# Kernel tuning notes

Hardware: AMD Instinct MI355X
Metric: run time of the kernel (lower is better)

## Reference

```python
import jax, jax.numpy as jnp
import numpy as np

NEG_FILL = -9.0e15
EPS = 1e-7


def setup_inputs() -> dict:
    key = jax.random.key(0)
    k1, k2, k3 = jax.random.split(key, 3)
    N, M, D = 8192, 8192, 256
    feat_x = jax.random.normal(k1, (N, D), dtype=jnp.float32)
    feat_y = jax.random.normal(k2, (M, D), dtype=jnp.float32)
    # Xavier-uniform init for W1 [in_dim, hidden_dim]
    limit = float(np.sqrt(6.0 / (D + D)))
    W1 = jax.random.uniform(k3, (D, D), dtype=jnp.float32, minval=-limit, maxval=limit)
    return {"feat_x": feat_x, "feat_y": feat_y, "W1": W1, "k": 32}


def reference(feat_x, feat_y, W1, k):
    # cosine-style normalization denominators
    norm1 = jnp.linalg.norm(feat_x, axis=1, keepdims=True)      # [N,1]
    norm2 = jnp.linalg.norm(feat_y, axis=1, keepdims=True)      # [M,1]
    # e = (X W1 Y^T) / (norm1 norm2^T + eps)   -> [N, M]
    e = (feat_x @ W1) @ feat_y.T
    e = e / (norm1 * norm2.T + EPS)
    # topk per row, scatter into -9e15-filled matrix, softmax over rows
    a, ind = jax.lax.top_k(e, k)                                # [N,k]
    A = jnp.full_like(e, NEG_FILL)
    rows = jnp.arange(e.shape[0])[:, None]
    A = A.at[rows, ind].set(a)
    attention = jax.nn.softmax(A, axis=1)
    return attention
```

## Files before the change

### kernel.cpp

```cpp
#include <hip/hip_runtime.h>
#include <hip/hip_bf16.h>
#include <stdint.h>

#define NROWS 8192
#define MCOLS 8192
#define DDIM  256
#define TOPK  32
#define NCHUNK 16
#define SEG   32
#define TAU 0.1375f

typedef __attribute__((ext_vector_type(8))) short short8;
typedef __attribute__((ext_vector_type(4))) float f32x4;
typedef __attribute__((ext_vector_type(4))) unsigned int u32x4;

__device__ __forceinline__ unsigned short f2bf(float x){
  __hip_bfloat16 h = __float2bfloat16(x);
  return *reinterpret_cast<unsigned short*>(&h);
}

__global__ __launch_bounds__(256,8) void prep_kernel(
    const float* __restrict__ X, const float* __restrict__ Y,
    float* __restrict__ n1, float* __restrict__ n2, float* __restrict__ rn2,
    unsigned short* __restrict__ Yb)
{
  int tid = threadIdx.x;
  int w = tid >> 6, lane = tid & 63;
  int row = blockIdx.x*4 + w;
  const float* src = (row < NROWS) ? (X + (size_t)row*DDIM) : (Y + (size_t)(row-NROWS)*DDIM);
  f32x4 v = ((const f32x4*)src)[lane];
  float s = v.x*v.x + v.y*v.y + v.z*v.z + v.w*v.w;
  #pragma unroll
  for (int off=32; off; off>>=1) s += __shfl_down(s, off);
  if (row < NROWS){
    if (lane==0) n1[row] = sqrtf(s);
  } else {
    int r = row - NROWS;
    if (lane==0){ float nn = sqrtf(s); n2[r] = nn; rn2[r] = 1.0f/nn; }
    ushort4 o; o.x=f2bf(v.x); o.y=f2bf(v.y); o.z=f2bf(v.z); o.w=f2bf(v.w);
    ((ushort4*)(Yb + (size_t)r*DDIM))[lane] = o;
  }
}

__global__ __launch_bounds__(256,4) void xp_kernel(
    const float* __restrict__ X, const float* __restrict__ W1,
    float* __restrict__ Xp, unsigned short* __restrict__ Xpb, float* __restrict__ t)
{
  __shared__ float Xs[8*DDIM];
  int tid = threadIdx.x;
  size_t rb = (size_t)blockIdx.x * 8;
  for (int i=tid; i<8*DDIM/4; i+=256) ((f32x4*)Xs)[i] = ((const f32x4*)(X + rb*DDIM))[i];
  __syncthreads();
  float acc[8]={0,0,0,0,0,0,0,0};
  int j = tid;
  for (int k=0;k<DDIM;k+=4){
    float w0 = W1[(k+0)*DDIM + j];
    float w1 = W1[(k+1)*DDIM + j];
    float w2 = W1[(k+2)*DDIM + j];
    float w3 = W1[(k+3)*DDIM + j];
    #pragma unroll
    for (int r=0;r<8;r++){
      f32x4 xv = *(const f32x4*)&Xs[r*DDIM + k];
      acc[r] = fmaf(xv.x, w0, acc[r]);
      acc[r] = fmaf(xv.y, w1, acc[r]);
      acc[r] = fmaf(xv.z, w2, acc[r]);
      acc[r] = fmaf(xv.w, w3, acc[r]);
    }
  }
  #pragma unroll
  for (int r=0;r<8;r++){
    float f = acc[r];
    size_t idx = (rb + r)*DDIM + j;
    Xp[idx]  = f;
    Xpb[idx] = f2bf(f);
  }
  __syncthreads();
  #pragma unroll
  for (int r=0;r<8;r++) Xs[r*DDIM + j] = acc[r]*acc[r];
  __syncthreads();
  int w = tid>>6, lane = tid&63;
  #pragma unroll
  for (int rr=0; rr<2; rr++){
    int r = w + rr*4;
    float s = Xs[r*DDIM + lane] + Xs[r*DDIM + lane + 64]
            + Xs[r*DDIM + lane + 128] + Xs[r*DDIM + lane + 192];
    #pragma unroll
    for (int off=32; off; off>>=1) s += __shfl_down(s, off);
    if (lane==0) t[rb + r] = TAU * sqrtf(s);
  }
}

__global__ __launch_bounds__(256,4) void cand_kernel(
    const unsigned short* __restrict__ Xpb, const unsigned short* __restrict__ Yb,
    const float* __restrict__ rn2, const float* __restrict__ t,
    unsigned int* __restrict__ cnt, uint2* __restrict__ cand)
{
  __shared__ unsigned short Bs[2][8192];
  __shared__ unsigned lcnt[64];
  int tid = threadIdx.x;
  int w = tid>>6, lane = tid&63;
  int quad = lane>>4, l16 = lane&15;
  int myrow = blockIdx.x*64 + w*16 + l16;
  int colchunk = blockIdx.y;

  if (tid < 64) lcnt[tid] = 0u;

  short8 a[8];
  #pragma unroll
  for (int kf=0; kf<8; kf++)
    a[kf] = *(const short8*)(Xpb + (size_t)myrow*DDIM + kf*32 + quad*8);
  float tv[4];
  #pragma unroll
  for (int rg=0;rg<4;rg++)
    tv[rg] = t[blockIdx.x*64 + w*16 + quad*4 + rg];

  u32x4 st[4];
  auto gload = [&](int ct, int kc){
    int colbase = colchunk*512 + ct*128;
    #pragma unroll
    for (int i=0;i<4;i++){
      int S = i*256 + tid;
      int c = S>>3, us = S&7;
      int ksrc = kc*64 + ((us ^ (c&7))<<3);
      st[i] = *(const u32x4*)(Yb + (size_t)(colbase + c)*DDIM + ksrc);
    }
  };
  gload(0,0);

  f32x4 acc[8];
  for (int ct=0; ct<4; ct++){
    #pragma unroll
    for (int nf=0;nf<8;nf++) acc[nf] = (f32x4){0.f,0.f,0.f,0.f};

    #pragma unroll
    for (int kc=0;kc<4;kc++){
      #pragma unroll
      for (int i=0;i<4;i++)
        ((u32x4*)&Bs[kc&1][0])[i*256 + tid] = st[i];
      __syncthreads();
      if (!(ct==3 && kc==3)){
        int nct = (kc<3)? ct : ct+1;
        int nkc = (kc<3)? kc+1 : 0;
        gload(nct, nkc);
      }
      #pragma unroll
      for (int kf=0;kf<2;kf++){
        #pragma unroll
        for (int nf=0;nf<8;nf++){
          int c = nf*16 + l16;
          int us = (kf*4+quad) ^ (c&7);
          short8 b = *(const short8*)&Bs[kc&1][c*64 + us*8];
          acc[nf] = __builtin_amdgcn_mfma_f32_16x16x32_bf16(a[kc*2+kf], b, acc[nf], 0,0,0);
        }
      }
    }
    int colbase = colchunk*512 + ct*128;
    #pragma unroll
    for (int nf=0;nf<8;nf++){
      float rv = rn2[colbase + nf*16 + l16];
      #pragma unroll
      for (int rg=0;rg<4;rg++){
        float sv = acc[nf][rg] * rv;
        if (sv > tv[rg]){
          int lr = w*16 + quad*4 + rg;
          unsigned slot = atomicAdd(&lcnt[lr], 1u);
          if (slot < SEG){
            size_t row = (size_t)blockIdx.x*64 + lr;
            cand[(row*NCHUNK + colchunk)*SEG + slot] =
              make_uint2(__float_as_uint(sv), (unsigned)(colbase + nf*16 + l16));
          }
        }
      }
    }
  }
  __syncthreads();
  if (tid < 64)
    cnt[((size_t)blockIdx.x*64 + tid)*NCHUNK + colchunk] = lcnt[tid];
}

__global__ __launch_bounds__(256,8) void refine_kernel(
    const float* __restrict__ Xp, const float* __restrict__ Y,
    const float* __restrict__ n1, const float* __restrict__ n2,
    const unsigned int* __restrict__ cnt, const uint2* __restrict__ cand,
    float* __restrict__ out)
{
  __shared__ float xs[DDIM];
  __shared__ unsigned pre[NCHUNK+1];
  __shared__ unsigned key32[256];
  __shared__ int ccol[256];
  __shared__ unsigned thr_s, scnt_s;
  __shared__ int scol[64];
  __shared__ double part[64][17];
  __shared__ double part2[64][5];
  __shared__ double exv[64];

  int row = blockIdx.x;
  int tid = threadIdx.x;
  int w = tid>>6, lane = tid&63;

  f32x4 z = {0.f,0.f,0.f,0.f};
  f32x4* orow = (f32x4*)(out + (size_t)row*MCOLS);
  #pragma unroll
  for (int i=0;i<8;i++) orow[tid + i*256] = z;

  if (tid < 64) ((f32x4*)xs)[tid] = ((const f32x4*)(Xp + (size_t)row*DDIM))[tid];
  if (tid < NCHUNK) pre[tid+1] = min(cnt[(size_t)row*NCHUNK + tid], (unsigned)SEG);
  if (tid == 0){ thr_s = 0u; scnt_s = 0u; }
  if (tid >= 64 && tid < 128) scol[tid-64] = 0;
  __syncthreads();
  if (tid == 0){
    pre[0] = 0;
    #pragma unroll
    for (int i=0;i<NCHUNK;i++) pre[i+1] += pre[i];
  }
  __syncthreads();
  int n = (int)min(pre[NCHUNK], 256u);
  unsigned myk = 0u; int mycol = 0;
  if (tid < n){
    int s = 0;
    while (s < NCHUNK-1 && (unsigned)tid >= pre[s+1]) s++;
    uint2 c = cand[((size_t)row*NCHUNK + s)*SEG + (tid - (int)pre[s])];
    myk = c.x; mycol = (int)c.y;
  }
  key32[tid] = myk;
  ccol[tid]  = mycol;
  __syncthreads();

  if (w == 0 && n > 64){
    unsigned k0 = key32[lane], k1 = key32[lane+64],
             k2 = key32[lane+128], k3 = key32[lane+192];
    unsigned lo = 0u, hi = 0xFFFFFFFFu;
    for (int it=0; it<25; ++it){
      unsigned mid = lo + ((hi - lo) >> 1);
      int c = __popcll(__ballot(k0 > mid)) + __popcll(__ballot(k1 > mid))
            + __popcll(__ballot(k2 > mid)) + __popcll(__ballot(k3 > mid));
      if (c >= 48 && c <= 64){ lo = mid; break; }
      if (c > 64) lo = mid; else hi = mid;
    }
    if (lane == 0) thr_s = lo;
  }
  __syncthreads();
  unsigned thr = thr_s;
  if (tid < n && myk > thr){
    unsigned s = atomicAdd(&scnt_s, 1u);
    if (s < 64) scol[s] = mycol;
  }
  __syncthreads();
  int scnt = (int)min(scnt_s, 64u);

  f32x4 xv = ((const f32x4*)xs)[lane];
  #pragma unroll
  for (int it=0; it<16; it++){
    int s = w + it*4;
    int col = scol[s];
    f32x4 yv = ((const f32x4*)(Y + (size_t)col*DDIM))[lane];
    double p = (double)xv.x*(double)yv.x + (double)xv.y*(double)yv.y
             + (double)xv.z*(double)yv.z + (double)xv.w*(double)yv.w;
    p += __shfl_down(p, 32);
    p += __shfl_down(p, 16);
    if (lane < 16) part[s][lane] = p;
  }
  __syncthreads();
  {
    int c = tid>>2, q = tid&3;
    if (c < 64){
      double s = part[c][q*4+0] + part[c][q*4+1] + part[c][q*4+2] + part[c][q*4+3];
      part2[c][q] = s;
    }
  }
  __syncthreads();
  if (tid < 64){
    double e = -1.0e300;
    if (tid < scnt){
      double s = part2[tid][0] + part2[tid][1] + part2[tid][2] + part2[tid][3];
      e = s / ((double)n1[row]*(double)n2[scol[tid]] + 1e-7);
    }
    exv[tid] = e;
  }
  __syncthreads();

  if (w == 0){
    double myv = exv[lane];
    int rank = 0;
    #pragma unroll 8
    for (int j=0;j<64;j++){
      double vj = exv[j];
      rank += (vj > myv) || (vj == myv && j < lane);
    }
    unsigned long long b = __ballot(rank == 0);
    int src = (int)(__ffsll((long long)b) - 1);
    double m = __shfl(myv, src);
    bool valid = (lane < scnt) && (rank < TOPK);
    double p = valid ? exp(myv - m) : 0.0;
    double ssum = p;
    #pragma unroll
    for (int off=32; off; off>>=1) ssum += __shfl_down(ssum, off);
    ssum = __shfl(ssum, 0);
    if (valid)
      out[(size_t)row*MCOLS + scol[lane]] = (float)(p/ssum);
  }
}

extern "C" void kernel_launch(void* const* d_in, const int* in_sizes, int n_in,
                              void* d_out, int out_size, void* d_ws, size_t ws_size,
                              hipStream_t stream)
{
  const float* X  = (const float*)d_in[0];
  const float* Y  = (const float*)d_in[1];
  const float* W1 = (const float*)d_in[2];
  float* out = (float*)d_out;

  char* ws = (char*)d_ws;
  float* n1  = (float*)(ws + 0);
  float* n2  = (float*)(ws + (32<<10));
  float* rn2 = (float*)(ws + (64<<10));
  float* t   = (float*)(ws + (96<<10));
  unsigned int* cnt = (unsigned int*)(ws + (128<<10));
  unsigned short* Yb  = (unsigned short*)(ws + (1u<<20));
  float* Xp = (float*)(ws + (5u<<20));
  unsigned short* Xpb = (unsigned short*)(ws + (13u<<20));
  uint2* cand = (uint2*)(ws + (17u<<20));

  hipLaunchKernelGGL(prep_kernel, dim3(4096), dim3(256), 0, stream, X, Y, n1, n2, rn2, Yb);
  hipLaunchKernelGGL(xp_kernel,   dim3(1024), dim3(256), 0, stream, X, W1, Xp, Xpb, t);
  hipLaunchKernelGGL(cand_kernel, dim3(128,16), dim3(256), 0, stream, Xpb, Yb, rn2, t, cnt, cand);
  hipLaunchKernelGGL(refine_kernel, dim3(8192), dim3(256), 0, stream, Xp, Y, n1, n2, cnt, cand, out);
}
```

Baseline: 476.6 us.

## Stage output row in LDS and write once; fold X norms into xp_kernel

The refine kernel no longer zero-fills its output row up front and then scatters up to 32 values into global memory. It builds the full row in a 32KB shared buffer, which aliases the scratch arrays, and streams it out with coalesced vector stores. Launch bounds drop to 4 blocks per CU to fit the larger shared memory. The X row norms are now computed inside xp_kernel from the tile it already loads, so prep_kernel only processes Y and launches half as many blocks. The cost is lower refine occupancy and an extra LDS pass over each row.

Measured after the change: 486.2 us. +2.0%, slower.

```diff
diff --git a/kernel.cpp b/kernel.cpp
--- a/kernel.cpp
+++ b/kernel.cpp
@@ -20,37 +20,43 @@
 }
 
 __global__ __launch_bounds__(256,8) void prep_kernel(
-    const float* __restrict__ X, const float* __restrict__ Y,
-    float* __restrict__ n1, float* __restrict__ n2, float* __restrict__ rn2,
+    const float* __restrict__ Y,
+    float* __restrict__ n2, float* __restrict__ rn2,
     unsigned short* __restrict__ Yb)
 {
   int tid = threadIdx.x;
   int w = tid >> 6, lane = tid & 63;
-  int row = blockIdx.x*4 + w;
-  const float* src = (row < NROWS) ? (X + (size_t)row*DDIM) : (Y + (size_t)(row-NROWS)*DDIM);
-  f32x4 v = ((const f32x4*)src)[lane];
+  int r = blockIdx.x*4 + w;
+  f32x4 v = ((const f32x4*)(Y + (size_t)r*DDIM))[lane];
   float s = v.x*v.x + v.y*v.y + v.z*v.z + v.w*v.w;
   #pragma unroll
   for (int off=32; off; off>>=1) s += __shfl_down(s, off);
-  if (row < NROWS){
-    if (lane==0) n1[row] = sqrtf(s);
-  } else {
-    int r = row - NROWS;
-    if (lane==0){ float nn = sqrtf(s); n2[r] = nn; rn2[r] = 1.0f/nn; }
-    ushort4 o; o.x=f2bf(v.x); o.y=f2bf(v.y); o.z=f2bf(v.z); o.w=f2bf(v.w);
-    ((ushort4*)(Yb + (size_t)r*DDIM))[lane] = o;
-  }
+  if (lane==0){ float nn = sqrtf(s); n2[r] = nn; rn2[r] = 1.0f/nn; }
+  ushort4 o; o.x=f2bf(v.x); o.y=f2bf(v.y); o.z=f2bf(v.z); o.w=f2bf(v.w);
+  ((ushort4*)(Yb + (size_t)r*DDIM))[lane] = o;
 }
 
 __global__ __launch_bounds__(256,4) void xp_kernel(
     const float* __restrict__ X, const float* __restrict__ W1,
-    float* __restrict__ Xp, unsigned short* __restrict__ Xpb, float* __restrict__ t)
+    float* __restrict__ Xp, unsigned short* __restrict__ Xpb,
+    float* __restrict__ t, float* __restrict__ n1)
 {
   __shared__ float Xs[8*DDIM];
   int tid = threadIdx.x;
+  int w = tid>>6, lane = tid&63;
   size_t rb = (size_t)blockIdx.x * 8;
   for (int i=tid; i<8*DDIM/4; i+=256) ((f32x4*)Xs)[i] = ((const f32x4*)(X + rb*DDIM))[i];
   __syncthreads();
+  #pragma unroll
+  for (int rr=0; rr<2; rr++){
+    int r = w + rr*4;
+    float x0 = Xs[r*DDIM + lane],       x1 = Xs[r*DDIM + lane + 64];
+    float x2 = Xs[r*DDIM + lane + 128], x3 = Xs[r*DDIM + lane + 192];
+    float s = x0*x0 + x1*x1 + x2*x2 + x3*x3;
+    #pragma unroll
+    for (int off=32; off; off>>=1) s += __shfl_down(s, off);
+    if (lane==0) n1[rb + r] = sqrtf(s);
+  }
   float acc[8]={0,0,0,0,0,0,0,0};
   int j = tid;
   for (int k=0;k<DDIM;k+=4){
@@ -78,7 +84,6 @@
   #pragma unroll
   for (int r=0;r<8;r++) Xs[r*DDIM + j] = acc[r]*acc[r];
   __syncthreads();
-  int w = tid>>6, lane = tid&63;
   #pragma unroll
   for (int rr=0; rr<2; rr++){
     int r = w + rr*4;
@@ -178,30 +183,28 @@
     cnt[((size_t)blockIdx.x*64 + tid)*NCHUNK + colchunk] = lcnt[tid];
 }
 
-__global__ __launch_bounds__(256,8) void refine_kernel(
+__global__ __launch_bounds__(256,4) void refine_kernel(
     const float* __restrict__ Xp, const float* __restrict__ Y,
     const float* __restrict__ n1, const float* __restrict__ n2,
     const unsigned int* __restrict__ cnt, const uint2* __restrict__ cand,
     float* __restrict__ out)
 {
+  __shared__ __align__(16) char smem[32768];
   __shared__ float xs[DDIM];
   __shared__ unsigned pre[NCHUNK+1];
-  __shared__ unsigned key32[256];
-  __shared__ int ccol[256];
   __shared__ unsigned thr_s, scnt_s;
   __shared__ int scol[64];
-  __shared__ double part[64][17];
-  __shared__ double part2[64][5];
   __shared__ double exv[64];
+
+  unsigned* key32 = (unsigned*)smem;
+  int* ccol       = (int*)(smem + 1024);
+  double (*part)[17]  = (double(*)[17])(smem + 2048);
+  double (*part2)[5]  = (double(*)[5])(smem + 2048+8704);
+  float* rowbuf   = (float*)smem;
 
   int row = blockIdx.x;
   int tid = threadIdx.x;
   int w = tid>>6, lane = tid&63;
-
-  f32x4 z = {0.f,0.f,0.f,0.f};
-  f32x4* orow = (f32x4*)(out + (size_t)row*MCOLS);
-  #pragma unroll
-  for (int i=0;i<8;i++) orow[tid + i*256] = z;
 
   if (tid < 64) ((f32x4*)xs)[tid] = ((const f32x4*)(Xp + (size_t)row*DDIM))[tid];
   if (tid < NCHUNK) pre[tid+1] = min(cnt[(size_t)row*NCHUNK + tid], (unsigned)SEG);
@@ -279,6 +282,7 @@
   }
   __syncthreads();
 
+  double pval = 0.0; int pcol = -1;
   if (w == 0){
     double myv = exv[lane];
     int rank = 0;
@@ -296,9 +300,24 @@
     #pragma unroll
     for (int off=32; off; off>>=1) ssum += __shfl_down(ssum, off);
     ssum = __shfl(ssum, 0);
-    if (valid)
-      out[(size_t)row*MCOLS + scol[lane]] = (float)(p/ssum);
-  }
+    if (valid){ pval = p/ssum; pcol = scol[lane]; }
+  } else {
+    f32x4 z = {0.f,0.f,0.f,0.f};
+    int t3 = tid - 64;
+    #pragma unroll
+    for (int i=0;i<11;i++){
+      int j = t3 + 192*i;
+      if (j < MCOLS/4) ((f32x4*)rowbuf)[j] = z;
+    }
+  }
+  __syncthreads();
+  if (w == 0 && lane < 64){
+    if (pcol >= 0) rowbuf[pcol] = (float)pval;
+  }
+  __syncthreads();
+  f32x4* orow = (f32x4*)(out + (size_t)row*MCOLS);
+  #pragma unroll
+  for (int i=0;i<8;i++) orow[tid + i*256] = ((f32x4*)rowbuf)[tid + i*256];
 }
 
 extern "C" void kernel_launch(void* const* d_in, const int* in_sizes, int n_in,
@@ -321,8 +340,8 @@
   unsigned short* Xpb = (unsigned short*)(ws + (13u<<20));
   uint2* cand = (uint2*)(ws + (17u<<20));
 
-  hipLaunchKernelGGL(prep_kernel, dim3(4096), dim3(256), 0, stream, X, Y, n1, n2, rn2, Yb);
-  hipLaunchKernelGGL(xp_kernel,   dim3(1024), dim3(256), 0, stream, X, W1, Xp, Xpb, t);
+  hipLaunchKernelGGL(prep_kernel, dim3(2048), dim3(256), 0, stream, Y, n2, rn2, Yb);
+  hipLaunchKernelGGL(xp_kernel,   dim3(1024), dim3(256), 0, stream, X, W1, Xp, Xpb, t, n1);
   hipLaunchKernelGGL(cand_kernel, dim3(128,16), dim3(256), 0, stream, Xpb, Yb, rn2, t, cnt, cand);
   hipLaunchKernelGGL(refine_kernel, dim3(8192), dim3(256), 0, stream, Xp, Y, n1, n2, cnt, cand, out);
 }
```
